# Kernel tuning notes

Hardware: AMD Instinct MI355X
Metric: run time of the kernel (lower is better)

Reference implementation:

```python
import jax, jax.numpy as jnp
import numpy as np

DIM = 768
HEADS = 12
HEAD_DIM = DIM // HEADS
B, N = 4, 2048


def setup_inputs() -> dict:
    key = jax.random.key(0)
    ks = jax.random.split(key, 5)
    s = 0.02
    return {
        "x": jax.random.normal(ks[0], (B, N, DIM), dtype=jnp.float32),
        "w_qkv": jax.random.normal(ks[1], (DIM, 3 * DIM), dtype=jnp.float32) * s,
        "b_qkv": jnp.zeros((3 * DIM,), dtype=jnp.float32),
        "w_proj": jax.random.normal(ks[2], (DIM, DIM), dtype=jnp.float32) * s,
        "b_proj": jnp.zeros((DIM,), dtype=jnp.float32),
    }


def reference(x, w_qkv, b_qkv, w_proj, b_proj):
    b, n, c = x.shape
    scale = HEAD_DIM ** -0.5
    qkv = x @ w_qkv + b_qkv                       # [B,N,3C]
    qkv = qkv.reshape(b, n, 3, HEADS, HEAD_DIM)
    q = qkv[:, :, 0].transpose(0, 2, 1, 3)        # [B,H,N,D]
    k = qkv[:, :, 1].transpose(0, 2, 1, 3)
    v = qkv[:, :, 2].transpose(0, 2, 1, 3)
    attn = jnp.einsum("bhqd,bhkd->bhqk", q, k) * scale
    attn = jax.nn.softmax(attn, axis=-1)
    out = jnp.einsum("bhqk,bhkd->bhqd", attn, v)  # [B,H,N,D]
    out = out.transpose(0, 2, 1, 3).reshape(b, n, c)
    return out @ w_proj + b_proj
```

## Files before the change

kernel.cpp:

```cpp
#include <hip/hip_runtime.h>

typedef short sh8 __attribute__((ext_vector_type(8)));
typedef short sh4 __attribute__((ext_vector_type(4)));
typedef float f32x4 __attribute__((ext_vector_type(4)));
typedef float f32x16 __attribute__((ext_vector_type(16)));
typedef unsigned u32x4 __attribute__((ext_vector_type(4)));

extern "C" __device__ float __ocml_native_exp2_f32(float);

__device__ __forceinline__ short f2bf(float f) {
  unsigned u = __builtin_bit_cast(unsigned, f);
  u += 0x7fffu + ((u >> 16) & 1u);
  return (short)(u >> 16);
}

__device__ __forceinline__ void gload16(const short* g, short* l) {
  __builtin_amdgcn_global_load_lds(
      (const __attribute__((address_space(1))) unsigned*)g,
      (__attribute__((address_space(3))) unsigned*)l, 16, 0, 0);
}

__device__ __forceinline__ void wait4_barrier() {
  asm volatile("s_waitcnt vmcnt(4)" ::: "memory");
  __builtin_amdgcn_s_barrier();
  asm volatile("" ::: "memory");
}
__device__ __forceinline__ void wait0_barrier() {
  asm volatile("s_waitcnt vmcnt(0)" ::: "memory");
  __builtin_amdgcn_s_barrier();
  asm volatile("" ::: "memory");
}

__global__ void cast_f32_bf16(const float* __restrict__ in, short* __restrict__ out, int n) {
  int i = (blockIdx.x * blockDim.x + threadIdx.x) * 4;
  if (i >= n) return;
  float4 f = *(const float4*)(in + i);
  sh4 o;
  o.x = f2bf(f.x); o.y = f2bf(f.y); o.z = f2bf(f.z); o.w = f2bf(f.w);
  *(sh4*)(out + i) = o;
}

__global__ void transpose_cast(const float* __restrict__ in, short* __restrict__ out, int K, int Nn) {
  int idx = blockIdx.x * blockDim.x + threadIdx.x;
  if (idx >= K * Nn) return;
  int k = idx / Nn;
  int n = idx - k * Nn;
  out[(size_t)n * K + k] = f2bf(in[idx]);
}

template <int OUTF32>
__global__ __launch_bounds__(256) void gemm_bt(
    const short* __restrict__ A, const short* __restrict__ Bt,
    const float* __restrict__ bias, void* __restrict__ Cv,
    int M, int Nn, int K) {
  __shared__ short As[3][128][32];
  __shared__ short Bs[3][128][32];
  const int t = threadIdx.x;
  const int wave = t >> 6, lane = t & 63, quad = lane >> 4, l15 = lane & 15;
  const int wm = (wave >> 1) * 64, wn = (wave & 1) * 64;
  const int row0 = blockIdx.y * 128, col0 = blockIdx.x * 128;
  f32x4 acc[4][4] = {};

  const int srow = t >> 2;
  const int ssl = ((t & 3) ^ ((t >> 3) & 3)) * 8;
  const short* Asrc0 = A + (size_t)(row0 + srow) * K + ssl;
  const short* Asrc1 = A + (size_t)(row0 + 64 + srow) * K + ssl;
  const short* Bsrc0 = Bt + (size_t)(col0 + srow) * K + ssl;
  const short* Bsrc1 = Bt + (size_t)(col0 + 64 + srow) * K + ssl;
  short* AsF = &As[0][0][0];
  short* BsF = &Bs[0][0][0];
  const int wdst = wave * 512;

  const int soA = (quad ^ ((l15 >> 1) & 3)) * 8;

  const int T = K >> 5;
#pragma unroll
  for (int pt = 0; pt < 2; pt++) {
    short* Ad = AsF + pt * 4096 + wdst;
    short* Bd = BsF + pt * 4096 + wdst;
    const int k0 = pt * 32;
    gload16(Asrc0 + k0, Ad);
    gload16(Asrc1 + k0, Ad + 2048);
    gload16(Bsrc0 + k0, Bd);
    gload16(Bsrc1 + k0, Bd + 2048);
  }

  int rb = 0, wb = 2;
  for (int tt = 0; tt < T; tt++) {
    if (tt + 1 < T) wait4_barrier(); else wait0_barrier();
    if (tt + 2 < T) {
      const int k0 = (tt + 2) * 32;
      short* Ad = AsF + wb * 4096 + wdst;
      short* Bd = BsF + wb * 4096 + wdst;
      gload16(Asrc0 + k0, Ad);
      gload16(Asrc1 + k0, Ad + 2048);
      gload16(Bsrc0 + k0, Bd);
      gload16(Bsrc1 + k0, Bd + 2048);
    }
    const short* Ab = AsF + rb * 4096;
    const short* Bb = BsF + rb * 4096;
    sh8 af[4], bfv[4];
#pragma unroll
    for (int i = 0; i < 4; i++) af[i] = *(const sh8*)&Ab[(wm + i * 16 + l15) * 32 + soA];
#pragma unroll
    for (int j = 0; j < 4; j++) bfv[j] = *(const sh8*)&Bb[(wn + j * 16 + l15) * 32 + soA];
#pragma unroll
    for (int i = 0; i < 4; i++)
#pragma unroll
      for (int j = 0; j < 4; j++)
        acc[i][j] = __builtin_amdgcn_mfma_f32_16x16x32_bf16(af[i], bfv[j], acc[i][j], 0, 0, 0);
    rb = rb == 2 ? 0 : rb + 1;
    wb = wb == 2 ? 0 : wb + 1;
  }

#pragma unroll
  for (int i = 0; i < 4; i++)
#pragma unroll
    for (int j = 0; j < 4; j++) {
      int r = row0 + wm + i * 16 + quad * 4;
      int c = col0 + wn + j * 16 + l15;
      float bv = bias[c];
#pragma unroll
      for (int e = 0; e < 4; e++) {
        float v = acc[i][j][e] + bv;
        if (OUTF32)
          ((float*)Cv)[(size_t)(r + e) * Nn + c] = v;
        else
          ((short*)Cv)[(size_t)(r + e) * Nn + c] = f2bf(v);
      }
    }
}

__global__ __launch_bounds__(256) void gemm_qkv(
    const short* __restrict__ A, const short* __restrict__ Bt,
    const float* __restrict__ bias,
    short* __restrict__ Qh, short* __restrict__ Kh, short* __restrict__ Vh) {
  const int K = 768;
  __shared__ short As[3][128][32];
  __shared__ short Bs[3][128][32];
  const int t = threadIdx.x;
  const int wave = t >> 6, lane = t & 63, quad = lane >> 4, l15 = lane & 15;
  const int wm = (wave >> 1) * 64, wn = (wave & 1) * 64;
  const int row0 = blockIdx.y * 128, col0 = blockIdx.x * 128;
  f32x4 acc[4][4] = {};

  const int srow = t >> 2;
  const int ssl = ((t & 3) ^ ((t >> 3) & 3)) * 8;
  const short* Asrc0 = A + (size_t)(row0 + srow) * K + ssl;
  const short* Asrc1 = A + (size_t)(row0 + 64 + srow) * K + ssl;
  const short* Bsrc0 = Bt + (size_t)(col0 + srow) * K + ssl;
  const short* Bsrc1 = Bt + (size_t)(col0 + 64 + srow) * K + ssl;
  short* AsF = &As[0][0][0];
  short* BsF = &Bs[0][0][0];
  const int wdst = wave * 512;

  const int soA = (quad ^ ((l15 >> 1) & 3)) * 8;

  const int T = K >> 5;
#pragma unroll
  for (int pt = 0; pt < 2; pt++) {
    short* Ad = AsF + pt * 4096 + wdst;
    short* Bd = BsF + pt * 4096 + wdst;
    const int k0 = pt * 32;
    gload16(Asrc0 + k0, Ad);
    gload16(Asrc1 + k0, Ad + 2048);
    gload16(Bsrc0 + k0, Bd);
    gload16(Bsrc1 + k0, Bd + 2048);
  }

  int rb = 0, wb = 2;
  for (int tt = 0; tt < T; tt++) {
    if (tt + 1 < T) wait4_barrier(); else wait0_barrier();
    if (tt + 2 < T) {
      const int k0 = (tt + 2) * 32;
      short* Ad = AsF + wb * 4096 + wdst;
      short* Bd = BsF + wb * 4096 + wdst;
      gload16(Asrc0 + k0, Ad);
      gload16(Asrc1 + k0, Ad + 2048);
      gload16(Bsrc0 + k0, Bd);
      gload16(Bsrc1 + k0, Bd + 2048);
    }
    const short* Ab = AsF + rb * 4096;
    const short* Bb = BsF + rb * 4096;
    sh8 af[4], bfv[4];
#pragma unroll
    for (int i = 0; i < 4; i++) af[i] = *(const sh8*)&Ab[(wm + i * 16 + l15) * 32 + soA];
#pragma unroll
    for (int j = 0; j < 4; j++) bfv[j] = *(const sh8*)&Bb[(wn + j * 16 + l15) * 32 + soA];
#pragma unroll
    for (int i = 0; i < 4; i++)
#pragma unroll
      for (int j = 0; j < 4; j++)
        acc[i][j] = __builtin_amdgcn_mfma_f32_16x16x32_bf16(af[i], bfv[j], acc[i][j], 0, 0, 0);
    rb = rb == 2 ? 0 : rb + 1;
    wb = wb == 2 ? 0 : wb + 1;
  }

  const int s = col0 >= 1536 ? 2 : (col0 >= 768 ? 1 : 0);
  short* dst = s == 0 ? Qh : (s == 1 ? Kh : Vh);
  const float scl = (s == 0) ? 0.18033688011112042f : 1.0f;

#pragma unroll
  for (int j = 0; j < 4; j++) {
    int c = col0 + wn + j * 16 + l15;
    int hd = c - s * 768;
    int h = hd >> 6;
    float bv = bias[c];
#pragma unroll
    for (int i = 0; i < 4; i++) {
      int rbase = row0 + wm + i * 16 + quad * 4;
#pragma unroll
      for (int e = 0; e < 4; e++) {
        int r = rbase + e;
        int b = r >> 11, n = r & 2047;
        float v = (acc[i][j][e] + bv) * scl;
        dst[(size_t)(b * 12 + h) * 131072 + n * 64 + (hd & 63)] = f2bf(v);
      }
    }
  }
}

__global__ __launch_bounds__(256) void transpose_v(const short* __restrict__ Vh,
                                                   short* __restrict__ VhT) {
  __shared__ short Tl[64][72];
  const int bid = blockIdx.x;
  const int bh = bid >> 5, nt = bid & 31;
  const size_t hb = (size_t)bh * 131072;
  const int t = threadIdx.x;
  const int r0 = t >> 3;
  const int c0 = (t & 7) * 8;
  sh8 a = *(const sh8*)&Vh[hb + (size_t)(nt * 64 + r0) * 64 + c0];
  sh8 b = *(const sh8*)&Vh[hb + (size_t)(nt * 64 + r0 + 32) * 64 + c0];
#pragma unroll
  for (int j = 0; j < 8; j++) Tl[c0 + j][r0] = a[j];
#pragma unroll
  for (int j = 0; j < 8; j++) Tl[c0 + j][r0 + 32] = b[j];
  __syncthreads();
  uint4 w0 = *(const uint4*)&Tl[r0][c0];
  uint4 w1 = *(const uint4*)&Tl[r0 + 32][c0];
  *(uint4*)&VhT[hb + (size_t)r0 * 2048 + nt * 64 + c0] = w0;
  *(uint4*)&VhT[hb + (size_t)(r0 + 32) * 2048 + nt * 64 + c0] = w1;
}

__global__ __launch_bounds__(256, 3) void attn7(const short* __restrict__ Qh,
                                                const short* __restrict__ Kh,
                                                const short* __restrict__ VhT,
                                                short* __restrict__ outb) {
  const int bid = blockIdx.x;
  const int qb = bid / 48;
  const int bh = bid - qb * 48;
  const int t = threadIdx.x;
  const int w = t >> 6, lane = t & 63;
  const int l31 = lane & 31, hi = lane >> 5;

  __shared__ short Kl[3][64][64];
  __shared__ short Vt[3][64][64];

  const size_t hb = (size_t)bh * 131072;

  sh8 qa[4];
  {
    const short* qp = Qh + hb + (size_t)(qb * 128 + w * 32 + l31) * 64 + hi * 8;
    qa[0] = *(const sh8*)(qp);
    qa[1] = *(const sh8*)(qp + 16);
    qa[2] = *(const sh8*)(qp + 32);
    qa[3] = *(const sh8*)(qp + 48);
  }
  asm volatile("s_waitcnt vmcnt(0)" ::: "memory");

  f32x16 o[2] = {};
  f32x4 lsv = {};

  const int srow = t >> 3;
  const int ssl = ((t & 7) ^ (srow & 7)) * 8;
  const short* Ksrc = Kh + hb + (size_t)srow * 64 + ssl;
  const short* Vsrc = VhT + hb + (size_t)srow * 2048 + ssl;
  short* KlF = &Kl[0][0][0];
  short* VtF = &Vt[0][0][0];
  const int wdst = w * 512;

  const int sw7 = l31 & 7;
  int rsl[4];
#pragma unroll
  for (int ks = 0; ks < 4; ks++) rsl[ks] = (((ks << 1) | hi) ^ sw7) * 8;

#pragma unroll
  for (int pt = 0; pt < 2; pt++) {
    const int key0 = pt * 64;
    short* Kd = KlF + pt * 4096 + wdst;
    short* Vd = VtF + pt * 4096 + wdst;
    gload16(Ksrc + (size_t)key0 * 64, Kd);
    gload16(Ksrc + (size_t)(key0 + 32) * 64, Kd + 2048);
    gload16(Vsrc + key0, Vd);
    gload16(Vsrc + (size_t)32 * 2048 + key0, Vd + 2048);
  }

  int rb = 0, wb = 2;
  for (int kt = 0; kt < 32; kt++) {
    if (kt < 31) wait4_barrier(); else wait0_barrier();
    if (kt < 30) {
      const int key0 = (kt + 2) * 64;
      short* Kd = KlF + wb * 4096 + wdst;
      short* Vd = VtF + wb * 4096 + wdst;
      gload16(Ksrc + (size_t)key0 * 64, Kd);
      gload16(Ksrc + (size_t)(key0 + 32) * 64, Kd + 2048);
      gload16(Vsrc + key0, Vd);
      gload16(Vsrc + (size_t)32 * 2048 + key0, Vd + 2048);
    }

    const short* Kb = KlF + rb * 4096;
    const short* Vb = VtF + rb * 4096;

    sh8 pa[4];
#pragma unroll
    for (int kb = 0; kb < 2; kb++) {
      const short* kr = Kb + (kb * 32 + l31) * 64;
      f32x16 s = {};
#pragma unroll
      for (int ks = 0; ks < 4; ks++)
        s = __builtin_amdgcn_mfma_f32_32x32x16_bf16(*(const sh8*)(kr + rsl[ks]), qa[ks], s, 0, 0, 0);
      unsigned u[8];
#pragma unroll
      for (int m = 0; m < 8; m++) {
        float e0 = __ocml_native_exp2_f32(s[2 * m]);
        float e1 = __ocml_native_exp2_f32(s[2 * m + 1]);
        lsv[m & 3] += e0 + e1;
        asm("v_cvt_pk_bf16_f32 %0, %1, %2" : "=v"(u[m]) : "v"(e0), "v"(e1));
      }
      unsigned y0 = (unsigned)__shfl_xor((int)(hi ? u[0] : u[2]), 32, 64);
      unsigned y1 = (unsigned)__shfl_xor((int)(hi ? u[1] : u[3]), 32, 64);
      unsigned y2 = (unsigned)__shfl_xor((int)(hi ? u[4] : u[6]), 32, 64);
      unsigned y3 = (unsigned)__shfl_xor((int)(hi ? u[5] : u[7]), 32, 64);
      unsigned w0 = hi ? y0 : u[0];
      unsigned w1 = hi ? y1 : u[1];
      unsigned w2 = hi ? u[2] : y0;
      unsigned w3 = hi ? u[3] : y1;
      unsigned w4 = hi ? y2 : u[4];
      unsigned w5 = hi ? y3 : u[5];
      unsigned w6 = hi ? u[6] : y2;
      unsigned w7 = hi ? u[7] : y3;
      u32x4 A0 = {w0, w1, w2, w3};
      u32x4 A1 = {w4, w5, w6, w7};
      pa[2 * kb] = __builtin_bit_cast(sh8, A0);
      pa[2 * kb + 1] = __builtin_bit_cast(sh8, A1);
    }

    __builtin_amdgcn_s_setprio(1);
#pragma unroll
    for (int db = 0; db < 2; db++) {
      const short* vr = Vb + (db * 32 + l31) * 64;
#pragma unroll
      for (int ks = 0; ks < 4; ks++)
        o[db] = __builtin_amdgcn_mfma_f32_32x32x16_bf16(pa[ks], *(const sh8*)(vr + rsl[ks]), o[db], 0, 0, 0);
    }
    __builtin_amdgcn_s_setprio(0);
    rb = rb == 2 ? 0 : rb + 1;
    wb = wb == 2 ? 0 : wb + 1;
  }

  float ls = lsv[0] + lsv[1] + lsv[2] + lsv[3];
  ls += __shfl_xor(ls, 32, 64);
  float inv = 1.f / ls;

  const int b = bh / 12, hh = bh - b * 12;
#pragma unroll
  for (int r = 0; r < 16; r++) {
    int qr = (r & 3) + 8 * (r >> 2) + 4 * hi;
    float iv = __shfl(inv, qr, 64);
    int n = qb * 128 + w * 32 + qr;
    short* op = outb + (size_t)(b * 2048 + n) * 768 + hh * 64 + l31;
    op[0] = f2bf(o[0][r] * iv);
    op[32] = f2bf(o[1][r] * iv);
  }
}

extern "C" void kernel_launch(void* const* d_in, const int* in_sizes, int n_in,
                              void* d_out, int out_size, void* d_ws, size_t ws_size,
                              hipStream_t stream) {
  const float* x = (const float*)d_in[0];
  const float* w_qkv = (const float*)d_in[1];
  const float* b_qkv = (const float*)d_in[2];
  const float* w_proj = (const float*)d_in[3];
  const float* b_proj = (const float*)d_in[4];
  float* out = (float*)d_out;

  char* p = (char*)d_ws;
  short* xb = (short*)p;     p += (size_t)8192 * 768 * 2;
  short* wqkvT = (short*)p;  p += (size_t)2304 * 768 * 2;
  short* wprojT = (short*)p; p += (size_t)768 * 768 * 2;
  short* Qh = (short*)p;     p += (size_t)48 * 131072 * 2;
  short* Kh = (short*)p;     p += (size_t)48 * 131072 * 2;
  short* Vh = (short*)p;     p += (size_t)48 * 131072 * 2;
  short* attnb = (short*)p;  p += (size_t)8192 * 768 * 2;
  short* VhT = xb;

  cast_f32_bf16<<<(8192 * 768 / 4) / 256, 256, 0, stream>>>(x, xb, 8192 * 768);
  transpose_cast<<<(768 * 2304 + 255) / 256, 256, 0, stream>>>(w_qkv, wqkvT, 768, 2304);
  transpose_cast<<<(768 * 768 + 255) / 256, 256, 0, stream>>>(w_proj, wprojT, 768, 768);

  dim3 g1(2304 / 128, 8192 / 128);
  gemm_qkv<<<g1, 256, 0, stream>>>(xb, wqkvT, b_qkv, Qh, Kh, Vh);

  transpose_v<<<48 * 32, 256, 0, stream>>>(Vh, VhT);

  attn7<<<16 * 48, 256, 0, stream>>>(Qh, Kh, VhT, attnb);

  dim3 g2(768 / 128, 8192 / 128);
  gemm_bt<1><<<g2, 256, 0, stream>>>(attnb, wprojT, b_proj, out, 8192, 768, 768);
}
```

Baseline: 245.0 us.

## Fuse V transpose into QKV GEMM epilogue, tile weight transposes, add XCD swizzle

The separate transpose_v kernel is removed. The QKV GEMM now writes V directly in transposed layout through an LDS staging tile, which saves a kernel launch and a round trip of V through global memory. The weight transpose-cast kernels become LDS-tiled with coalesced float4 reads and 16-byte writes, replacing the old strided scalar stores. Both GEMMs also remap block IDs with an XCD-aware swizzle so neighbouring tiles share L2, at the cost of some extra index arithmetic and one more LDS pass in the V epilogue.

```diff
diff --git a/kernel.cpp b/kernel.cpp
--- a/kernel.cpp
+++ b/kernel.cpp
@@ -29,6 +29,12 @@
   asm volatile("s_waitcnt vmcnt(0)" ::: "memory");
   __builtin_amdgcn_s_barrier();
   asm volatile("" ::: "memory");
+}
+
+__device__ __forceinline__ int xcd_swizzle(int bidl, int nwg) {
+  int q = nwg >> 3, rr = nwg & 7;
+  int xcd = bidl & 7, idx = bidl >> 3;
+  return (xcd < rr ? xcd * (q + 1) : rr * (q + 1) + (xcd - rr) * q) + idx;
 }
 
 __global__ void cast_f32_bf16(const float* __restrict__ in, short* __restrict__ out, int n) {
@@ -40,12 +46,30 @@
   *(sh4*)(out + i) = o;
 }
 
-__global__ void transpose_cast(const float* __restrict__ in, short* __restrict__ out, int K, int Nn) {
-  int idx = blockIdx.x * blockDim.x + threadIdx.x;
-  if (idx >= K * Nn) return;
-  int k = idx / Nn;
-  int n = idx - k * Nn;
-  out[(size_t)n * K + k] = f2bf(in[idx]);
+__global__ __launch_bounds__(256) void transpose_cast_t(
+    const float* __restrict__ in, short* __restrict__ out, int K, int Nn) {
+  __shared__ short Tl[64][72];
+  const int t = threadIdx.x;
+  const int n0 = blockIdx.x * 64, k0 = blockIdx.y * 64;
+  const int kr0 = t >> 4;
+  const int nc = (t & 15) * 4;
+#pragma unroll
+  for (int p = 0; p < 4; p++) {
+    int kr = kr0 + p * 16;
+    float4 f = *(const float4*)(in + (size_t)(k0 + kr) * Nn + n0 + nc);
+    Tl[nc + 0][kr] = f2bf(f.x);
+    Tl[nc + 1][kr] = f2bf(f.y);
+    Tl[nc + 2][kr] = f2bf(f.z);
+    Tl[nc + 3][kr] = f2bf(f.w);
+  }
+  __syncthreads();
+  const int nr0 = t >> 3;
+  const int kk = (t & 7) * 8;
+#pragma unroll
+  for (int p = 0; p < 2; p++) {
+    int nr = nr0 + p * 32;
+    *(sh8*)(out + (size_t)(n0 + nr) * K + k0 + kk) = *(const sh8*)&Tl[nr][kk];
+  }
 }
 
 template <int OUTF32>
@@ -58,7 +82,9 @@
   const int t = threadIdx.x;
   const int wave = t >> 6, lane = t & 63, quad = lane >> 4, l15 = lane & 15;
   const int wm = (wave >> 1) * 64, wn = (wave & 1) * 64;
-  const int row0 = blockIdx.y * 128, col0 = blockIdx.x * 128;
+  const int nwg = gridDim.x * gridDim.y;
+  const int wg = xcd_swizzle(blockIdx.y * gridDim.x + blockIdx.x, nwg);
+  const int row0 = (wg / gridDim.x) * 128, col0 = (wg % gridDim.x) * 128;
   f32x4 acc[4][4] = {};
 
   const int srow = t >> 2;
@@ -134,14 +160,15 @@
 __global__ __launch_bounds__(256) void gemm_qkv(
     const short* __restrict__ A, const short* __restrict__ Bt,
     const float* __restrict__ bias,
-    short* __restrict__ Qh, short* __restrict__ Kh, short* __restrict__ Vh) {
+    short* __restrict__ Qh, short* __restrict__ Kh, short* __restrict__ VhT) {
   const int K = 768;
-  __shared__ short As[3][128][32];
-  __shared__ short Bs[3][128][32];
+  __shared__ short SMEM[24576];
   const int t = threadIdx.x;
   const int wave = t >> 6, lane = t & 63, quad = lane >> 4, l15 = lane & 15;
   const int wm = (wave >> 1) * 64, wn = (wave & 1) * 64;
-  const int row0 = blockIdx.y * 128, col0 = blockIdx.x * 128;
+  const int nwg = gridDim.x * gridDim.y;
+  const int wg = xcd_swizzle(blockIdx.y * gridDim.x + blockIdx.x, nwg);
+  const int row0 = (wg / gridDim.x) * 128, col0 = (wg % gridDim.x) * 128;
   f32x4 acc[4][4] = {};
 
   const int srow = t >> 2;
@@ -150,8 +177,8 @@
   const short* Asrc1 = A + (size_t)(row0 + 64 + srow) * K + ssl;
   const short* Bsrc0 = Bt + (size_t)(col0 + srow) * K + ssl;
   const short* Bsrc1 = Bt + (size_t)(col0 + 64 + srow) * K + ssl;
-  short* AsF = &As[0][0][0];
-  short* BsF = &Bs[0][0][0];
+  short* AsF = SMEM;
+  short* BsF = SMEM + 12288;
   const int wdst = wave * 512;
 
   const int soA = (quad ^ ((l15 >> 1) & 3)) * 8;
@@ -197,49 +224,57 @@
   }
 
   const int s = col0 >= 1536 ? 2 : (col0 >= 768 ? 1 : 0);
-  short* dst = s == 0 ? Qh : (s == 1 ? Kh : Vh);
-  const float scl = (s == 0) ? 0.18033688011112042f : 1.0f;
-
-#pragma unroll
-  for (int j = 0; j < 4; j++) {
-    int c = col0 + wn + j * 16 + l15;
-    int hd = c - s * 768;
-    int h = hd >> 6;
-    float bv = bias[c];
-#pragma unroll
-    for (int i = 0; i < 4; i++) {
-      int rbase = row0 + wm + i * 16 + quad * 4;
-#pragma unroll
-      for (int e = 0; e < 4; e++) {
-        int r = rbase + e;
-        int b = r >> 11, n = r & 2047;
-        float v = (acc[i][j][e] + bv) * scl;
-        dst[(size_t)(b * 12 + h) * 131072 + n * 64 + (hd & 63)] = f2bf(v);
+
+  if (s < 2) {
+    short* dst = s == 0 ? Qh : Kh;
+    const float scl = (s == 0) ? 0.18033688011112042f : 1.0f;
+#pragma unroll
+    for (int j = 0; j < 4; j++) {
+      int c = col0 + wn + j * 16 + l15;
+      int hd = c - s * 768;
+      int h = hd >> 6;
+      float bv = bias[c];
+#pragma unroll
+      for (int i = 0; i < 4; i++) {
+        int rbase = row0 + wm + i * 16 + quad * 4;
+#pragma unroll
+        for (int e = 0; e < 4; e++) {
+          int r = rbase + e;
+          int b = r >> 11, n = r & 2047;
+          float v = (acc[i][j][e] + bv) * scl;
+          dst[(size_t)(b * 12 + h) * 131072 + n * 64 + (hd & 63)] = f2bf(v);
+        }
       }
     }
-  }
-}
-
-__global__ __launch_bounds__(256) void transpose_v(const short* __restrict__ Vh,
-                                                   short* __restrict__ VhT) {
-  __shared__ short Tl[64][72];
-  const int bid = blockIdx.x;
-  const int bh = bid >> 5, nt = bid & 31;
-  const size_t hb = (size_t)bh * 131072;
-  const int t = threadIdx.x;
-  const int r0 = t >> 3;
-  const int c0 = (t & 7) * 8;
-  sh8 a = *(const sh8*)&Vh[hb + (size_t)(nt * 64 + r0) * 64 + c0];
-  sh8 b = *(const sh8*)&Vh[hb + (size_t)(nt * 64 + r0 + 32) * 64 + c0];
-#pragma unroll
-  for (int j = 0; j < 8; j++) Tl[c0 + j][r0] = a[j];
-#pragma unroll
-  for (int j = 0; j < 8; j++) Tl[c0 + j][r0 + 32] = b[j];
-  __syncthreads();
-  uint4 w0 = *(const uint4*)&Tl[r0][c0];
-  uint4 w1 = *(const uint4*)&Tl[r0 + 32][c0];
-  *(uint4*)&VhT[hb + (size_t)r0 * 2048 + nt * 64 + c0] = w0;
-  *(uint4*)&VhT[hb + (size_t)(r0 + 32) * 2048 + nt * 64 + c0] = w1;
+  } else {
+    __syncthreads();
+    short* Tl = SMEM;
+#pragma unroll
+    for (int j = 0; j < 4; j++) {
+      int cl = wn + j * 16 + l15;
+      float bv = bias[col0 + cl];
+#pragma unroll
+      for (int i = 0; i < 4; i++) {
+        int rl = wm + i * 16 + quad * 4;
+        sh4 pk;
+#pragma unroll
+        for (int e = 0; e < 4; e++) pk[e] = f2bf(acc[i][j][e] + bv);
+        *(sh4*)&Tl[cl * 136 + rl] = pk;
+      }
+    }
+    __syncthreads();
+    const int b = row0 >> 11, n0 = row0 & 2047;
+    const int h0 = (col0 - 1536) >> 6;
+#pragma unroll
+    for (int p = 0; p < 8; p++) {
+      int cl = (t >> 4) + p * 16;
+      int nn = (t & 15) * 8;
+      int hg = h0 + (cl >> 6);
+      int d = cl & 63;
+      sh8 vv = *(const sh8*)&Tl[cl * 136 + nn];
+      *(sh8*)&VhT[(size_t)(b * 12 + hg) * 131072 + (size_t)d * 2048 + n0 + nn] = vv;
+    }
+  }
 }
 
 __global__ __launch_bounds__(256, 3) void attn7(const short* __restrict__ Qh,
@@ -390,18 +425,21 @@
   short* wprojT = (short*)p; p += (size_t)768 * 768 * 2;
   short* Qh = (short*)p;     p += (size_t)48 * 131072 * 2;
   short* Kh = (short*)p;     p += (size_t)48 * 131072 * 2;
-  short* Vh = (short*)p;     p += (size_t)48 * 131072 * 2;
+  short* VhT = (short*)p;    p += (size_t)48 * 131072 * 2;
   short* attnb = (short*)p;  p += (size_t)8192 * 768 * 2;
-  short* VhT = xb;
 
   cast_f32_bf16<<<(8192 * 768 / 4) / 256, 256, 0, stream>>>(x, xb, 8192 * 768);
-  transpose_cast<<<(768 * 2304 + 255) / 256, 256, 0, stream>>>(w_qkv, wqkvT, 768, 2304);
-  transpose_cast<<<(768 * 768 + 255) / 256, 256, 0, stream>>>(w_proj, wprojT, 768, 768);
+  {
+    dim3 gt(2304 / 64, 768 / 64);
+    transpose_cast_t<<<gt, 256, 0, stream>>>(w_qkv, wqkvT, 768, 2304);
+  }
+  {
+    dim3 gt(768 / 64, 768 / 64);
+    transpose_cast_t<<<gt, 256, 0, stream>>>(w_proj, wprojT, 768, 768);
+  }
 
   dim3 g1(2304 / 128, 8192 / 128);
-  gemm_qkv<<<g1, 256, 0, stream>>>(xb, wqkvT, b_qkv, Qh, Kh, Vh);
-
-  transpose_v<<<48 * 32, 256, 0, stream>>>(Vh, VhT);
+  gemm_qkv<<<g1, 256, 0, stream>>>(xb, wqkvT, b_qkv, Qh, Kh, VhT);
 
   attn7<<<16 * 48, 256, 0, stream>>>(Qh, Kh, VhT, attnb);
 
```

After: 223.8 us. 8.6% less time.
